# Kernel optimization log

Measured on AMD Instinct MI355X. Metric: run time of the kernel, lower is better.

The kernel has to match this reference:

```python
import jax, jax.numpy as jnp
import numpy as np

HID = 2048
TAU_MIN, TAU_MAX, DT, SPARSITY = 1.0, 20.0, 0.5, 0.15
LN_EPS = 1e-5


def setup_inputs() -> dict:
    key = jax.random.key(0)
    ks = jax.random.split(key, 6)
    B, S, H = 16, 512, HID
    x = jax.random.normal(ks[0], (B, S, H), jnp.float32)
    # input_projection: Linear(H, H) (kaiming-uniform-ish scale)
    Wi = jax.random.normal(ks[1], (H, H), jnp.float32) * (1.0 / np.sqrt(H))
    b = jnp.zeros((H,), jnp.float32)
    # recurrent weights, xavier_normal gain=2.0, then sparsified by fixed mask
    Wr = jax.random.normal(ks[2], (H, H), jnp.float32) * (2.0 * np.sqrt(2.0 / (H + H)))
    mask = (jax.random.uniform(ks[3], (H, H)) < SPARSITY).astype(jnp.float32)
    Wr = Wr * mask
    # tau ~ exp(U(log tau_min, log tau_max))
    log_tau = jax.random.uniform(ks[4], (H,)) * (np.log(TAU_MAX) - np.log(TAU_MIN)) + np.log(TAU_MIN)
    tau = jnp.exp(log_tau).astype(jnp.float32)
    gamma = jnp.ones((H,), jnp.float32)
    beta = jnp.zeros((H,), jnp.float32)
    return {"x": x, "Wi": Wi, "b": b, "Wr": Wr, "mask": mask, "tau": tau, "gamma": gamma, "beta": beta}


def reference(x, Wi, b, Wr, mask, tau, gamma, beta):
    # x: [B, S, H]
    B, S, H = x.shape
    # input projection for all timesteps at once (math-equivalent to per-step Linear)
    inp = jnp.einsum('bsh,oh->bso', x, Wi) + b  # [B, S, H]
    Wm = Wr * mask                              # masked recurrent weights [H, H]
    tau_c = jnp.clip(tau, TAU_MIN, TAU_MAX)
    alpha = jnp.clip(DT / tau_c, 0.0, 1.0)      # [H]

    def step(state, inp_t):
        # state: [B, H], inp_t: [B, H]
        target = jnp.tanh(inp_t + state @ Wm.T)
        state = jnp.clip(state + alpha * (target - state), -1.0, 1.0)
        return state, state

    state0 = jnp.zeros((B, H), x.dtype)
    _, outs = jax.lax.scan(step, state0, jnp.swapaxes(inp, 0, 1))  # [S, B, H]
    outs = jnp.swapaxes(outs, 0, 1)  # [B, S, H]
    # LayerNorm over last dim (biased variance, as torch)
    mu = outs.mean(-1, keepdims=True)
    var = ((outs - mu) ** 2).mean(-1, keepdims=True)
    return (outs - mu) * jax.lax.rsqrt(var + LN_EPS) * gamma + beta
```

## Files before the change

### kernel.cpp

```cpp
#include <hip/hip_runtime.h>
#include <math.h>

typedef __bf16 bf16_t;
typedef __bf16 bf16x8 __attribute__((ext_vector_type(8)));
typedef float f32x4 __attribute__((ext_vector_type(4)));
typedef int i32x4 __attribute__((ext_vector_type(4)));
typedef unsigned int u32;

#define HID 2048
#define NBATCH 16
#define SEQLEN 512
#define MTOT (NBATCH * SEQLEN)
#define NBLK 32
#define RTHREADS 256
#define LN_EPS 1e-5f

__global__ __launch_bounds__(256) void gemm_proj(
    const float* __restrict__ X,
    const float* __restrict__ Wi,
    const float* __restrict__ bias,
    float* __restrict__ C,
    int* __restrict__ flags)
{
    __shared__ bf16_t lA[128 * 32];
    __shared__ bf16_t lB[128 * 32];
    const int tid = threadIdx.x;
    if (blockIdx.x == 0 && blockIdx.y == 0) {
        if (tid < NBLK) flags[tid] = 0;
    }
    const int lane = tid & 63;
    const int wv = tid >> 6;
    const int bn = blockIdx.x * 128;
    const int bm = blockIdx.y * 128;
    const int wr = (wv >> 1) * 64;
    const int wc = (wv & 1) * 64;

    f32x4 zero = {0.f, 0.f, 0.f, 0.f};
    f32x4 acc[4][4];
#pragma unroll
    for (int i = 0; i < 4; ++i)
#pragma unroll
        for (int j = 0; j < 4; ++j) acc[i][j] = zero;

    for (int k0 = 0; k0 < HID; k0 += 32) {
        __syncthreads();
#pragma unroll
        for (int c = 0; c < 2; ++c) {
            const int chunk = c * 256 + tid;
            const int row = chunk >> 2;
            const int kp = (chunk & 3) ^ (row & 3);
            {
                const float* s = X + (size_t)(bm + row) * HID + k0 + kp * 8;
                float4 a0 = *(const float4*)s;
                float4 a1 = *(const float4*)(s + 4);
                bf16x8 v;
                v[0] = (bf16_t)a0.x; v[1] = (bf16_t)a0.y; v[2] = (bf16_t)a0.z; v[3] = (bf16_t)a0.w;
                v[4] = (bf16_t)a1.x; v[5] = (bf16_t)a1.y; v[6] = (bf16_t)a1.z; v[7] = (bf16_t)a1.w;
                *(bf16x8*)(lA + chunk * 8) = v;
            }
            {
                const float* s = Wi + (size_t)(bn + row) * HID + k0 + kp * 8;
                float4 a0 = *(const float4*)s;
                float4 a1 = *(const float4*)(s + 4);
                bf16x8 v;
                v[0] = (bf16_t)a0.x; v[1] = (bf16_t)a0.y; v[2] = (bf16_t)a0.z; v[3] = (bf16_t)a0.w;
                v[4] = (bf16_t)a1.x; v[5] = (bf16_t)a1.y; v[6] = (bf16_t)a1.z; v[7] = (bf16_t)a1.w;
                *(bf16x8*)(lB + chunk * 8) = v;
            }
        }
        __syncthreads();

        bf16x8 af[4], bfr[4];
#pragma unroll
        for (int i = 0; i < 4; ++i) {
            const int row = wr + i * 16 + (lane & 15);
            const int ck = (lane >> 4) ^ (row & 3);
            af[i] = *(const bf16x8*)(lA + row * 32 + ck * 8);
        }
#pragma unroll
        for (int j = 0; j < 4; ++j) {
            const int row = wc + j * 16 + (lane & 15);
            const int ck = (lane >> 4) ^ (row & 3);
            bfr[j] = *(const bf16x8*)(lB + row * 32 + ck * 8);
        }
#pragma unroll
        for (int i = 0; i < 4; ++i)
#pragma unroll
            for (int j = 0; j < 4; ++j)
                acc[i][j] = __builtin_amdgcn_mfma_f32_16x16x32_bf16(af[i], bfr[j], acc[i][j], 0, 0, 0);
    }

#pragma unroll
    for (int j = 0; j < 4; ++j) {
        const int col = bn + wc + j * 16 + (lane & 15);
        const float bv = bias[col];
#pragma unroll
        for (int i = 0; i < 4; ++i) {
#pragma unroll
            for (int r = 0; r < 4; ++r) {
                const int row = bm + wr + i * 16 + (lane >> 4) * 4 + r;
                C[(size_t)row * HID + col] = acc[i][j][r] + bv;
            }
        }
    }
}

__global__ __launch_bounds__(RTHREADS, 1) void recurrent(
    const float* __restrict__ Wr,
    const float* __restrict__ mask,
    const float* __restrict__ tau,
    float* __restrict__ io,
    bf16_t* __restrict__ st0,
    bf16_t* __restrict__ st1,
    int* __restrict__ flags)
{
    const int tid = threadIdx.x;
    const int lane = tid & 63;
    const int wv = tid >> 6;
    const int colbase = blockIdx.x * 64;

    __shared__ float red[4][16][68];

    bf16x8 wf[64];
    {
        const int kb = wv * 512 + (lane >> 4) * 8;
#pragma unroll
        for (int ct = 0; ct < 4; ++ct) {
            const int gc = colbase + ct * 16 + (lane & 15);
#pragma unroll
            for (int kf = 0; kf < 16; ++kf) {
                const size_t off = (size_t)gc * HID + kb + kf * 32;
                float4 a0 = *(const float4*)(Wr + off);
                float4 a1 = *(const float4*)(Wr + off + 4);
                float4 m0 = *(const float4*)(mask + off);
                float4 m1 = *(const float4*)(mask + off + 4);
                bf16x8 v;
                v[0] = (bf16_t)(a0.x * m0.x); v[1] = (bf16_t)(a0.y * m0.y);
                v[2] = (bf16_t)(a0.z * m0.z); v[3] = (bf16_t)(a0.w * m0.w);
                v[4] = (bf16_t)(a1.x * m1.x); v[5] = (bf16_t)(a1.y * m1.y);
                v[6] = (bf16_t)(a1.z * m1.z); v[7] = (bf16_t)(a1.w * m1.w);
                wf[ct * 16 + kf] = v;
            }
        }
    }

    const int row = tid >> 4;
    const int cg  = (tid & 15) * 4;
    const int gcol = colbase + cg;
    float al[4];
#pragma unroll
    for (int j = 0; j < 4; ++j) {
        float tv = tau[gcol + j];
        tv = fminf(fmaxf(tv, 1.0f), 20.0f);
        al[j] = fminf(fmaxf(0.5f / tv, 0.0f), 1.0f);
    }

    float s_old[4] = {0.f, 0.f, 0.f, 0.f};
    union F4 { float4 v; float f[4]; };
    F4 cin; cin.v = *(const float4*)(io + (size_t)row * (SEQLEN * HID) + gcol);

    const int akb = wv * 512 + (lane >> 4) * 8;
    bf16_t* cur = st0;
    bf16_t* nxt = st1;

    {
        float sn[4]; F4 ov;
#pragma unroll
        for (int j = 0; j < 4; ++j) {
            float z = fminf(fmaxf(cin.f[j], -15.f), 15.f);
            const float e = __expf(2.0f * z);
            const float tg = (e - 1.0f) / (e + 1.0f);
            float s = al[j] * tg;
            s = fminf(fmaxf(s, -1.0f), 1.0f);
            sn[j] = s; ov.f[j] = s;
        }
        union { bf16_t b[2]; u32 u; } p0, p1;
        p0.b[0] = (bf16_t)sn[0]; p0.b[1] = (bf16_t)sn[1];
        p1.b[0] = (bf16_t)sn[2]; p1.b[1] = (bf16_t)sn[3];
        u32* sp = (u32*)(nxt + (size_t)row * HID + gcol);
        __hip_atomic_store(sp,     p0.u, __ATOMIC_RELAXED, __HIP_MEMORY_SCOPE_AGENT);
        __hip_atomic_store(sp + 1, p1.u, __ATOMIC_RELAXED, __HIP_MEMORY_SCOPE_AGENT);
        *(float4*)(io + (size_t)row * (SEQLEN * HID) + gcol) = ov.v;
#pragma unroll
        for (int j = 0; j < 4; ++j) s_old[j] = sn[j];
        cin.v = *(const float4*)(io + (size_t)row * (SEQLEN * HID) + HID + gcol);
        bf16_t* tmp = cur; cur = nxt; nxt = tmp;
    }

    for (int t = 1; t < SEQLEN; ++t) {
        __syncthreads();
        if (tid == 0)
            __hip_atomic_store(flags + (int)blockIdx.x, t,
                               __ATOMIC_RELAXED, __HIP_MEMORY_SCOPE_AGENT);
        if (wv == 0) {
            int v;
            do {
                v = __hip_atomic_load(flags + (lane & 31),
                                      __ATOMIC_RELAXED, __HIP_MEMORY_SCOPE_AGENT);
            } while (__ballot(v < t) != 0ull);
        }
        __syncthreads();

        const bf16_t* ab = cur + (size_t)(lane & 15) * HID + akb;
        union uf { i32x4 i; bf16x8 v; } a[16];
        asm volatile("global_load_dwordx4 %0, %1, off sc0 sc1"            : "=v"(a[0].i)  : "v"(ab) : "memory");
        asm volatile("global_load_dwordx4 %0, %1, off offset:64 sc0 sc1"  : "=v"(a[1].i)  : "v"(ab) : "memory");
        asm volatile("global_load_dwordx4 %0, %1, off offset:128 sc0 sc1" : "=v"(a[2].i)  : "v"(ab) : "memory");
        asm volatile("global_load_dwordx4 %0, %1, off offset:192 sc0 sc1" : "=v"(a[3].i)  : "v"(ab) : "memory");
        asm volatile("global_load_dwordx4 %0, %1, off offset:256 sc0 sc1" : "=v"(a[4].i)  : "v"(ab) : "memory");
        asm volatile("global_load_dwordx4 %0, %1, off offset:320 sc0 sc1" : "=v"(a[5].i)  : "v"(ab) : "memory");
        asm volatile("global_load_dwordx4 %0, %1, off offset:384 sc0 sc1" : "=v"(a[6].i)  : "v"(ab) : "memory");
        asm volatile("global_load_dwordx4 %0, %1, off offset:448 sc0 sc1" : "=v"(a[7].i)  : "v"(ab) : "memory");
        asm volatile("global_load_dwordx4 %0, %1, off offset:512 sc0 sc1" : "=v"(a[8].i)  : "v"(ab) : "memory");
        asm volatile("global_load_dwordx4 %0, %1, off offset:576 sc0 sc1" : "=v"(a[9].i)  : "v"(ab) : "memory");
        asm volatile("global_load_dwordx4 %0, %1, off offset:640 sc0 sc1" : "=v"(a[10].i) : "v"(ab) : "memory");
        asm volatile("global_load_dwordx4 %0, %1, off offset:704 sc0 sc1" : "=v"(a[11].i) : "v"(ab) : "memory");
        asm volatile("global_load_dwordx4 %0, %1, off offset:768 sc0 sc1" : "=v"(a[12].i) : "v"(ab) : "memory");
        asm volatile("global_load_dwordx4 %0, %1, off offset:832 sc0 sc1" : "=v"(a[13].i) : "v"(ab) : "memory");
        asm volatile("global_load_dwordx4 %0, %1, off offset:896 sc0 sc1" : "=v"(a[14].i) : "v"(ab) : "memory");
        asm volatile("global_load_dwordx4 %0, %1, off offset:960 sc0 sc1" : "=v"(a[15].i) : "v"(ab) : "memory");

        f32x4 acc0 = {0.f,0.f,0.f,0.f}, acc1 = {0.f,0.f,0.f,0.f};
        f32x4 acc2 = {0.f,0.f,0.f,0.f}, acc3 = {0.f,0.f,0.f,0.f};

        asm volatile("s_waitcnt vmcnt(8)" ::: "memory");
        __builtin_amdgcn_sched_barrier(0);
#define MF(kf) \
        acc0 = __builtin_amdgcn_mfma_f32_16x16x32_bf16(a[kf].v, wf[kf],      acc0, 0, 0, 0); \
        acc1 = __builtin_amdgcn_mfma_f32_16x16x32_bf16(a[kf].v, wf[16 + kf], acc1, 0, 0, 0); \
        acc2 = __builtin_amdgcn_mfma_f32_16x16x32_bf16(a[kf].v, wf[32 + kf], acc2, 0, 0, 0); \
        acc3 = __builtin_amdgcn_mfma_f32_16x16x32_bf16(a[kf].v, wf[48 + kf], acc3, 0, 0, 0);
        MF(0) MF(1) MF(2) MF(3) MF(4) MF(5) MF(6) MF(7)
        asm volatile("s_waitcnt vmcnt(0)" ::: "memory");
        __builtin_amdgcn_sched_barrier(0);
        MF(8) MF(9) MF(10) MF(11) MF(12) MF(13) MF(14) MF(15)
#undef MF

        {
            const int r0 = (lane >> 4) * 4;
            const int cA = lane & 15;
#pragma unroll
            for (int r = 0; r < 4; ++r) {
                red[wv][r0 + r][cA]      = acc0[r];
                red[wv][r0 + r][16 + cA] = acc1[r];
                red[wv][r0 + r][32 + cA] = acc2[r];
                red[wv][r0 + r][48 + cA] = acc3[r];
            }
        }
        __syncthreads();

        F4 s0, s1, s2, s3;
        s0.v = *(const float4*)&red[0][row][cg];
        s1.v = *(const float4*)&red[1][row][cg];
        s2.v = *(const float4*)&red[2][row][cg];
        s3.v = *(const float4*)&red[3][row][cg];

        float sn[4]; F4 ov;
#pragma unroll
        for (int j = 0; j < 4; ++j) {
            const float rec = s0.f[j] + s1.f[j] + s2.f[j] + s3.f[j];
            float z = cin.f[j] + rec;
            z = fminf(fmaxf(z, -15.f), 15.f);
            const float e = __expf(2.0f * z);
            const float tg = (e - 1.0f) / (e + 1.0f);
            float s = s_old[j] + al[j] * (tg - s_old[j]);
            s = fminf(fmaxf(s, -1.0f), 1.0f);
            sn[j] = s; ov.f[j] = s;
        }

        union { bf16_t b[2]; u32 u; } p0, p1;
        p0.b[0] = (bf16_t)sn[0]; p0.b[1] = (bf16_t)sn[1];
        p1.b[0] = (bf16_t)sn[2]; p1.b[1] = (bf16_t)sn[3];
        u32* sp = (u32*)(nxt + (size_t)row * HID + gcol);
        __hip_atomic_store(sp,     p0.u, __ATOMIC_RELAXED, __HIP_MEMORY_SCOPE_AGENT);
        __hip_atomic_store(sp + 1, p1.u, __ATOMIC_RELAXED, __HIP_MEMORY_SCOPE_AGENT);

        *(float4*)(io + (size_t)row * (SEQLEN * HID) + (size_t)t * HID + gcol) = ov.v;
        const int tn = (t < SEQLEN - 1) ? (t + 1) : t;
        cin.v = *(const float4*)(io + (size_t)row * (SEQLEN * HID) + (size_t)tn * HID + gcol);
#pragma unroll
        for (int j = 0; j < 4; ++j) s_old[j] = sn[j];
        bf16_t* tmp = cur; cur = nxt; nxt = tmp;
    }
}

__global__ __launch_bounds__(256) void ln_kernel(
    float* __restrict__ io,
    const float* __restrict__ gamma,
    const float* __restrict__ beta)
{
    const size_t row = blockIdx.x;
    float* p = io + row * HID;
    const int tid = threadIdx.x;
    float4 v0 = *(const float4*)(p + tid * 4);
    float4 v1 = *(const float4*)(p + 1024 + tid * 4);
    float s  = v0.x + v0.y + v0.z + v0.w + v1.x + v1.y + v1.z + v1.w;
    float ss = v0.x * v0.x + v0.y * v0.y + v0.z * v0.z + v0.w * v0.w
             + v1.x * v1.x + v1.y * v1.y + v1.z * v1.z + v1.w * v1.w;
#pragma unroll
    for (int off = 32; off > 0; off >>= 1) {
        s  += __shfl_down(s, off, 64);
        ss += __shfl_down(ss, off, 64);
    }
    __shared__ float rs[4], rss[4];
    if ((tid & 63) == 0) { rs[tid >> 6] = s; rss[tid >> 6] = ss; }
    __syncthreads();
    s  = rs[0] + rs[1] + rs[2] + rs[3];
    ss = rss[0] + rss[1] + rss[2] + rss[3];
    const float mu = s * (1.f / HID);
    const float var = ss * (1.f / HID) - mu * mu;
    const float inv = rsqrtf(var + LN_EPS);
    const int c0 = tid * 4, c1 = 1024 + tid * 4;
    float4 g0 = *(const float4*)(gamma + c0);
    float4 g1 = *(const float4*)(gamma + c1);
    float4 b0 = *(const float4*)(beta + c0);
    float4 b1 = *(const float4*)(beta + c1);
    float4 o0, o1;
    o0.x = (v0.x - mu) * inv * g0.x + b0.x;
    o0.y = (v0.y - mu) * inv * g0.y + b0.y;
    o0.z = (v0.z - mu) * inv * g0.z + b0.z;
    o0.w = (v0.w - mu) * inv * g0.w + b0.w;
    o1.x = (v1.x - mu) * inv * g1.x + b1.x;
    o1.y = (v1.y - mu) * inv * g1.y + b1.y;
    o1.z = (v1.z - mu) * inv * g1.z + b1.z;
    o1.w = (v1.w - mu) * inv * g1.w + b1.w;
    *(float4*)(p + tid * 4) = o0;
    *(float4*)(p + 1024 + tid * 4) = o1;
}

extern "C" void kernel_launch(void* const* d_in, const int* in_sizes, int n_in,
                              void* d_out, int out_size, void* d_ws, size_t ws_size,
                              hipStream_t stream)
{
    const float* x     = (const float*)d_in[0];
    const float* Wi    = (const float*)d_in[1];
    const float* bias  = (const float*)d_in[2];
    const float* Wr    = (const float*)d_in[3];
    const float* mask  = (const float*)d_in[4];
    const float* tau   = (const float*)d_in[5];
    const float* gamma = (const float*)d_in[6];
    const float* beta  = (const float*)d_in[7];
    float* out = (float*)d_out;

    bf16_t* st0 = (bf16_t*)d_ws;
    bf16_t* st1 = st0 + (size_t)NBATCH * HID;
    int* flags  = (int*)(st1 + (size_t)NBATCH * HID);

    gemm_proj<<<dim3(16, 64), 256, 0, stream>>>(x, Wi, bias, out, flags);
    recurrent<<<NBLK, RTHREADS, 0, stream>>>(Wr, mask, tau, out, st0, st1, flags);
    ln_kernel<<<MTOT, 256, 0, stream>>>(out, gamma, beta);
}
```

Baseline: 2.223 ms.

## Split recurrent K-reduction over 8 waves and publish step flag right after store

The recurrent kernel now runs 8 waves per block instead of 4. Each wave holds half as many weight fragments and issues half as many state loads and MFMAs per step, and an 8-way LDS reduction replaces the 4-way one. The step flag is now raised at the end of each iteration, after a vmcnt(0) wait and a raw s_barrier, instead of at the top of the next iteration. The next step's input is also prefetched alongside the state loads. The goal is to shorten the per-step critical path of the serial recurrence, at the cost of more LDS traffic and more lanes in each barrier.

After: 2.346 ms. +5.5%, slower.

```diff
diff --git a/kernel.cpp b/kernel.cpp
--- a/kernel.cpp
+++ b/kernel.cpp
@@ -12,7 +12,7 @@
 #define SEQLEN 512
 #define MTOT (NBATCH * SEQLEN)
 #define NBLK 32
-#define RTHREADS 256
+#define RTHREADS 512
 #define LN_EPS 1e-5f
 
 __global__ __launch_bounds__(256) void gemm_proj(
@@ -119,16 +119,16 @@
     const int wv = tid >> 6;
     const int colbase = blockIdx.x * 64;
 
-    __shared__ float red[4][16][68];
-
-    bf16x8 wf[64];
+    __shared__ float red[8][16][68];
+
+    bf16x8 wf[32];
     {
-        const int kb = wv * 512 + (lane >> 4) * 8;
+        const int kb = wv * 256 + (lane >> 4) * 8;
 #pragma unroll
         for (int ct = 0; ct < 4; ++ct) {
             const int gc = colbase + ct * 16 + (lane & 15);
 #pragma unroll
-            for (int kf = 0; kf < 16; ++kf) {
+            for (int kf = 0; kf < 8; ++kf) {
                 const size_t off = (size_t)gc * HID + kb + kf * 32;
                 float4 a0 = *(const float4*)(Wr + off);
                 float4 a1 = *(const float4*)(Wr + off + 4);
@@ -139,59 +139,51 @@
                 v[2] = (bf16_t)(a0.z * m0.z); v[3] = (bf16_t)(a0.w * m0.w);
                 v[4] = (bf16_t)(a1.x * m1.x); v[5] = (bf16_t)(a1.y * m1.y);
                 v[6] = (bf16_t)(a1.z * m1.z); v[7] = (bf16_t)(a1.w * m1.w);
-                wf[ct * 16 + kf] = v;
-            }
-        }
-    }
-
-    const int row = tid >> 4;
-    const int cg  = (tid & 15) * 4;
-    const int gcol = colbase + cg;
-    float al[4];
-#pragma unroll
-    for (int j = 0; j < 4; ++j) {
-        float tv = tau[gcol + j];
-        tv = fminf(fmaxf(tv, 1.0f), 20.0f);
-        al[j] = fminf(fmaxf(0.5f / tv, 0.0f), 1.0f);
-    }
-
-    float s_old[4] = {0.f, 0.f, 0.f, 0.f};
-    union F4 { float4 v; float f[4]; };
-    F4 cin; cin.v = *(const float4*)(io + (size_t)row * (SEQLEN * HID) + gcol);
-
-    const int akb = wv * 512 + (lane >> 4) * 8;
+                wf[ct * 8 + kf] = v;
+            }
+        }
+    }
+
+    const int row = tid >> 5;
+    const int uc  = (tid & 31) * 2;
+    const int gcol = colbase + uc;
+    float al0, al1;
+    {
+        float tv0 = fminf(fmaxf(tau[gcol],     1.0f), 20.0f);
+        float tv1 = fminf(fmaxf(tau[gcol + 1], 1.0f), 20.0f);
+        al0 = fminf(fmaxf(0.5f / tv0, 0.0f), 1.0f);
+        al1 = fminf(fmaxf(0.5f / tv1, 0.0f), 1.0f);
+    }
+
+    float s_old0 = 0.f, s_old1 = 0.f;
+    float2 cin = *(const float2*)(io + (size_t)row * (SEQLEN * HID) + gcol);
+
+    const int akb = wv * 256 + (lane >> 4) * 8;
     bf16_t* cur = st0;
     bf16_t* nxt = st1;
 
     {
-        float sn[4]; F4 ov;
-#pragma unroll
-        for (int j = 0; j < 4; ++j) {
-            float z = fminf(fmaxf(cin.f[j], -15.f), 15.f);
-            const float e = __expf(2.0f * z);
-            const float tg = (e - 1.0f) / (e + 1.0f);
-            float s = al[j] * tg;
-            s = fminf(fmaxf(s, -1.0f), 1.0f);
-            sn[j] = s; ov.f[j] = s;
-        }
-        union { bf16_t b[2]; u32 u; } p0, p1;
-        p0.b[0] = (bf16_t)sn[0]; p0.b[1] = (bf16_t)sn[1];
-        p1.b[0] = (bf16_t)sn[2]; p1.b[1] = (bf16_t)sn[3];
-        u32* sp = (u32*)(nxt + (size_t)row * HID + gcol);
-        __hip_atomic_store(sp,     p0.u, __ATOMIC_RELAXED, __HIP_MEMORY_SCOPE_AGENT);
-        __hip_atomic_store(sp + 1, p1.u, __ATOMIC_RELAXED, __HIP_MEMORY_SCOPE_AGENT);
-        *(float4*)(io + (size_t)row * (SEQLEN * HID) + gcol) = ov.v;
-#pragma unroll
-        for (int j = 0; j < 4; ++j) s_old[j] = sn[j];
-        cin.v = *(const float4*)(io + (size_t)row * (SEQLEN * HID) + HID + gcol);
-        bf16_t* tmp = cur; cur = nxt; nxt = tmp;
-    }
-
-    for (int t = 1; t < SEQLEN; ++t) {
+        float z0 = fminf(fmaxf(cin.x, -15.f), 15.f);
+        float z1 = fminf(fmaxf(cin.y, -15.f), 15.f);
+        const float e0 = __expf(2.0f * z0), e1 = __expf(2.0f * z1);
+        float sn0 = fminf(fmaxf(al0 * ((e0 - 1.0f) / (e0 + 1.0f)), -1.0f), 1.0f);
+        float sn1 = fminf(fmaxf(al1 * ((e1 - 1.0f) / (e1 + 1.0f)), -1.0f), 1.0f);
+        union { bf16_t b[2]; u32 u; } p;
+        p.b[0] = (bf16_t)sn0; p.b[1] = (bf16_t)sn1;
+        __hip_atomic_store((u32*)(nxt + (size_t)row * HID + gcol), p.u,
+                           __ATOMIC_RELAXED, __HIP_MEMORY_SCOPE_AGENT);
+        float2 ov; ov.x = sn0; ov.y = sn1;
+        *(float2*)(io + (size_t)row * (SEQLEN * HID) + gcol) = ov;
+        s_old0 = sn0; s_old1 = sn1;
+        cin = *(const float2*)(io + (size_t)row * (SEQLEN * HID) + HID + gcol);
         __syncthreads();
         if (tid == 0)
-            __hip_atomic_store(flags + (int)blockIdx.x, t,
+            __hip_atomic_store(flags + (int)blockIdx.x, 1,
                                __ATOMIC_RELAXED, __HIP_MEMORY_SCOPE_AGENT);
+        bf16_t* tmp = cur; cur = nxt; nxt = tmp;
+    }
+
+    for (int t = 1; t < SEQLEN; ++t) {
         if (wv == 0) {
             int v;
             do {
@@ -199,41 +191,37 @@
                                       __ATOMIC_RELAXED, __HIP_MEMORY_SCOPE_AGENT);
             } while (__ballot(v < t) != 0ull);
         }
-        __syncthreads();
+        __builtin_amdgcn_sched_barrier(0);
+        asm volatile("s_barrier" ::: "memory");
+        __builtin_amdgcn_sched_barrier(0);
 
         const bf16_t* ab = cur + (size_t)(lane & 15) * HID + akb;
-        union uf { i32x4 i; bf16x8 v; } a[16];
-        asm volatile("global_load_dwordx4 %0, %1, off sc0 sc1"            : "=v"(a[0].i)  : "v"(ab) : "memory");
-        asm volatile("global_load_dwordx4 %0, %1, off offset:64 sc0 sc1"  : "=v"(a[1].i)  : "v"(ab) : "memory");
-        asm volatile("global_load_dwordx4 %0, %1, off offset:128 sc0 sc1" : "=v"(a[2].i)  : "v"(ab) : "memory");
-        asm volatile("global_load_dwordx4 %0, %1, off offset:192 sc0 sc1" : "=v"(a[3].i)  : "v"(ab) : "memory");
-        asm volatile("global_load_dwordx4 %0, %1, off offset:256 sc0 sc1" : "=v"(a[4].i)  : "v"(ab) : "memory");
-        asm volatile("global_load_dwordx4 %0, %1, off offset:320 sc0 sc1" : "=v"(a[5].i)  : "v"(ab) : "memory");
-        asm volatile("global_load_dwordx4 %0, %1, off offset:384 sc0 sc1" : "=v"(a[6].i)  : "v"(ab) : "memory");
-        asm volatile("global_load_dwordx4 %0, %1, off offset:448 sc0 sc1" : "=v"(a[7].i)  : "v"(ab) : "memory");
-        asm volatile("global_load_dwordx4 %0, %1, off offset:512 sc0 sc1" : "=v"(a[8].i)  : "v"(ab) : "memory");
-        asm volatile("global_load_dwordx4 %0, %1, off offset:576 sc0 sc1" : "=v"(a[9].i)  : "v"(ab) : "memory");
-        asm volatile("global_load_dwordx4 %0, %1, off offset:640 sc0 sc1" : "=v"(a[10].i) : "v"(ab) : "memory");
-        asm volatile("global_load_dwordx4 %0, %1, off offset:704 sc0 sc1" : "=v"(a[11].i) : "v"(ab) : "memory");
-        asm volatile("global_load_dwordx4 %0, %1, off offset:768 sc0 sc1" : "=v"(a[12].i) : "v"(ab) : "memory");
-        asm volatile("global_load_dwordx4 %0, %1, off offset:832 sc0 sc1" : "=v"(a[13].i) : "v"(ab) : "memory");
-        asm volatile("global_load_dwordx4 %0, %1, off offset:896 sc0 sc1" : "=v"(a[14].i) : "v"(ab) : "memory");
-        asm volatile("global_load_dwordx4 %0, %1, off offset:960 sc0 sc1" : "=v"(a[15].i) : "v"(ab) : "memory");
+        union uf { i32x4 i; bf16x8 v; } a0_, a1_, a2_, a3_, a4_, a5_, a6_, a7_;
+        asm volatile("global_load_dwordx4 %0, %1, off sc0 sc1"            : "=v"(a0_.i) : "v"(ab) : "memory");
+        asm volatile("global_load_dwordx4 %0, %1, off offset:64 sc0 sc1"  : "=v"(a1_.i) : "v"(ab) : "memory");
+        asm volatile("global_load_dwordx4 %0, %1, off offset:128 sc0 sc1" : "=v"(a2_.i) : "v"(ab) : "memory");
+        asm volatile("global_load_dwordx4 %0, %1, off offset:192 sc0 sc1" : "=v"(a3_.i) : "v"(ab) : "memory");
+        asm volatile("global_load_dwordx4 %0, %1, off offset:256 sc0 sc1" : "=v"(a4_.i) : "v"(ab) : "memory");
+        asm volatile("global_load_dwordx4 %0, %1, off offset:320 sc0 sc1" : "=v"(a5_.i) : "v"(ab) : "memory");
+        asm volatile("global_load_dwordx4 %0, %1, off offset:384 sc0 sc1" : "=v"(a6_.i) : "v"(ab) : "memory");
+        asm volatile("global_load_dwordx4 %0, %1, off offset:448 sc0 sc1" : "=v"(a7_.i) : "v"(ab) : "memory");
+        const int tn = (t < SEQLEN - 1) ? (t + 1) : t;
+        float2 cin_next = *(const float2*)(io + (size_t)row * (SEQLEN * HID) + (size_t)tn * HID + gcol);
 
         f32x4 acc0 = {0.f,0.f,0.f,0.f}, acc1 = {0.f,0.f,0.f,0.f};
         f32x4 acc2 = {0.f,0.f,0.f,0.f}, acc3 = {0.f,0.f,0.f,0.f};
 
-        asm volatile("s_waitcnt vmcnt(8)" ::: "memory");
-        __builtin_amdgcn_sched_barrier(0);
-#define MF(kf) \
-        acc0 = __builtin_amdgcn_mfma_f32_16x16x32_bf16(a[kf].v, wf[kf],      acc0, 0, 0, 0); \
-        acc1 = __builtin_amdgcn_mfma_f32_16x16x32_bf16(a[kf].v, wf[16 + kf], acc1, 0, 0, 0); \
-        acc2 = __builtin_amdgcn_mfma_f32_16x16x32_bf16(a[kf].v, wf[32 + kf], acc2, 0, 0, 0); \
-        acc3 = __builtin_amdgcn_mfma_f32_16x16x32_bf16(a[kf].v, wf[48 + kf], acc3, 0, 0, 0);
-        MF(0) MF(1) MF(2) MF(3) MF(4) MF(5) MF(6) MF(7)
-        asm volatile("s_waitcnt vmcnt(0)" ::: "memory");
-        __builtin_amdgcn_sched_barrier(0);
-        MF(8) MF(9) MF(10) MF(11) MF(12) MF(13) MF(14) MF(15)
+        asm volatile("s_waitcnt vmcnt(5)" ::: "memory");
+        __builtin_amdgcn_sched_barrier(0);
+#define MF(u_, kf) \
+        acc0 = __builtin_amdgcn_mfma_f32_16x16x32_bf16(u_.v, wf[kf],      acc0, 0, 0, 0); \
+        acc1 = __builtin_amdgcn_mfma_f32_16x16x32_bf16(u_.v, wf[8 + kf],  acc1, 0, 0, 0); \
+        acc2 = __builtin_amdgcn_mfma_f32_16x16x32_bf16(u_.v, wf[16 + kf], acc2, 0, 0, 0); \
+        acc3 = __builtin_amdgcn_mfma_f32_16x16x32_bf16(u_.v, wf[24 + kf], acc3, 0, 0, 0);
+        MF(a0_, 0) MF(a1_, 1) MF(a2_, 2) MF(a3_, 3)
+        asm volatile("s_waitcnt vmcnt(1)" ::: "memory");
+        __builtin_amdgcn_sched_barrier(0);
+        MF(a4_, 4) MF(a5_, 5) MF(a6_, 6) MF(a7_, 7)
 #undef MF
 
         {
@@ -247,39 +235,43 @@
                 red[wv][r0 + r][48 + cA] = acc3[r];
             }
         }
-        __syncthreads();
-
-        F4 s0, s1, s2, s3;
-        s0.v = *(const float4*)&red[0][row][cg];
-        s1.v = *(const float4*)&red[1][row][cg];
-        s2.v = *(const float4*)&red[2][row][cg];
-        s3.v = *(const float4*)&red[3][row][cg];
-
-        float sn[4]; F4 ov;
-#pragma unroll
-        for (int j = 0; j < 4; ++j) {
-            const float rec = s0.f[j] + s1.f[j] + s2.f[j] + s3.f[j];
-            float z = cin.f[j] + rec;
-            z = fminf(fmaxf(z, -15.f), 15.f);
-            const float e = __expf(2.0f * z);
-            const float tg = (e - 1.0f) / (e + 1.0f);
-            float s = s_old[j] + al[j] * (tg - s_old[j]);
-            s = fminf(fmaxf(s, -1.0f), 1.0f);
-            sn[j] = s; ov.f[j] = s;
-        }
-
-        union { bf16_t b[2]; u32 u; } p0, p1;
-        p0.b[0] = (bf16_t)sn[0]; p0.b[1] = (bf16_t)sn[1];
-        p1.b[0] = (bf16_t)sn[2]; p1.b[1] = (bf16_t)sn[3];
-        u32* sp = (u32*)(nxt + (size_t)row * HID + gcol);
-        __hip_atomic_store(sp,     p0.u, __ATOMIC_RELAXED, __HIP_MEMORY_SCOPE_AGENT);
-        __hip_atomic_store(sp + 1, p1.u, __ATOMIC_RELAXED, __HIP_MEMORY_SCOPE_AGENT);
-
-        *(float4*)(io + (size_t)row * (SEQLEN * HID) + (size_t)t * HID + gcol) = ov.v;
-        const int tn = (t < SEQLEN - 1) ? (t + 1) : t;
-        cin.v = *(const float4*)(io + (size_t)row * (SEQLEN * HID) + (size_t)tn * HID + gcol);
-#pragma unroll
-        for (int j = 0; j < 4; ++j) s_old[j] = sn[j];
+        asm volatile("s_waitcnt lgkmcnt(0)" ::: "memory");
+        __builtin_amdgcn_sched_barrier(0);
+        asm volatile("s_barrier" ::: "memory");
+        __builtin_amdgcn_sched_barrier(0);
+
+        float rec0 = 0.f, rec1 = 0.f;
+#pragma unroll
+        for (int q = 0; q < 8; ++q) {
+            float2 s = *(const float2*)&red[q][row][uc];
+            rec0 += s.x; rec1 += s.y;
+        }
+
+        float z0 = fminf(fmaxf(cin.x + rec0, -15.f), 15.f);
+        float z1 = fminf(fmaxf(cin.y + rec1, -15.f), 15.f);
+        const float e0 = __expf(2.0f * z0), e1 = __expf(2.0f * z1);
+        const float tg0 = (e0 - 1.0f) / (e0 + 1.0f);
+        const float tg1 = (e1 - 1.0f) / (e1 + 1.0f);
+        float sn0 = fminf(fmaxf(s_old0 + al0 * (tg0 - s_old0), -1.0f), 1.0f);
+        float sn1 = fminf(fmaxf(s_old1 + al1 * (tg1 - s_old1), -1.0f), 1.0f);
+
+        union { bf16_t b[2]; u32 u; } p;
+        p.b[0] = (bf16_t)sn0; p.b[1] = (bf16_t)sn1;
+        __hip_atomic_store((u32*)(nxt + (size_t)row * HID + gcol), p.u,
+                           __ATOMIC_RELAXED, __HIP_MEMORY_SCOPE_AGENT);
+        float2 ov; ov.x = sn0; ov.y = sn1;
+        *(float2*)(io + (size_t)row * (SEQLEN * HID) + (size_t)t * HID + gcol) = ov;
+
+        asm volatile("s_waitcnt vmcnt(0)" ::: "memory");
+        __builtin_amdgcn_sched_barrier(0);
+        asm volatile("s_barrier" ::: "memory");
+        __builtin_amdgcn_sched_barrier(0);
+        if (t != SEQLEN - 1 && tid == 0)
+            __hip_atomic_store(flags + (int)blockIdx.x, t + 1,
+                               __ATOMIC_RELAXED, __HIP_MEMORY_SCOPE_AGENT);
+
+        s_old0 = sn0; s_old1 = sn1;
+        cin = cin_next;
         bf16_t* tmp = cur; cur = nxt; nxt = tmp;
     }
 }
```
